# Performance work log

Hardware: AMD Instinct MI355X
Metric: run time of the kernel (lower is better)

Reference implementation:

```python
import jax, jax.numpy as jnp
import numpy as np

N = 20000      # nodes (single node type)
E = 320000     # edges per relation (avg degree 16)
R = 3          # relations / edge types
L = 3          # layers
H = 4          # heads
D = 64         # dim per head (hid_size // n_heads)
IN = 256       # in_size == hid_size
OUT = 128      # out_size
NEG_SLOPE = 0.2


def setup_inputs() -> dict:
    key = jax.random.key(0)
    ks = jax.random.split(key, 8)
    x = jax.random.normal(ks[0], (N, IN), jnp.float32)
    edge_src = jax.random.randint(ks[1], (R, E), 0, N, dtype=jnp.int32)
    edge_dst = jax.random.randint(ks[2], (R, E), 0, N, dtype=jnp.int32)
    W = jax.random.normal(ks[3], (L, R, IN, H * D), jnp.float32) * (1.0 / np.sqrt(IN))
    attn_l = jax.random.normal(ks[4], (L, R, H, D), jnp.float32) * 0.1
    attn_r = jax.random.normal(ks[5], (L, R, H, D), jnp.float32) * 0.1
    bias = jnp.zeros((L, R, H * D), jnp.float32)
    fc_w = jax.random.normal(ks[6], (IN, OUT), jnp.float32) * (1.0 / np.sqrt(IN))
    fc_b = jnp.zeros((OUT,), jnp.float32)
    return dict(x=x, edge_src=edge_src, edge_dst=edge_dst, W=W,
                attn_l=attn_l, attn_r=attn_r, bias=bias, fc_w=fc_w, fc_b=fc_b)


def _gat_conv(h, src, dst, W_r, al, ar, b_r):
    # h: [N, IN] -> feat: [N, H, D]
    feat = (h @ W_r).reshape(N, H, D)
    el = jnp.sum(feat * al, axis=-1)                      # [N, H]
    er = jnp.sum(feat * ar, axis=-1)                      # [N, H]
    e = jax.nn.leaky_relu(el[src] + er[dst], NEG_SLOPE)   # [E, H]
    # segment softmax over incoming edges of each dst node, per head
    m = jax.ops.segment_max(e, dst, num_segments=N)       # [N, H]
    a = jnp.exp(e - m[dst])
    s = jax.ops.segment_sum(a, dst, num_segments=N)       # [N, H]
    alpha = a / s[dst]                                    # [E, H]
    # weighted scatter-add of source features: [N, H, D]
    out = jax.ops.segment_sum(alpha[:, :, None] * feat[src], dst, num_segments=N)
    return out + b_r.reshape(1, H, D)


def reference(x, edge_src, edge_dst, W, attn_l, attn_r, bias, fc_w, fc_b):
    h = x
    for l in range(L):
        acc = jnp.zeros((N, H, D), h.dtype)
        for r in range(R):  # sum-aggregate across relations (HeteroGraphConv aggregate='sum')
            acc = acc + _gat_conv(h, edge_src[r], edge_dst[r],
                                  W[l, r], attn_l[l, r], attn_r[l, r], bias[l, r])
        h = acc.reshape(N, H * D)
        if l != L - 1:
            h = jax.nn.relu(h)  # dropout = identity in eval
    return h @ fc_w + fc_b  # [N, OUT]
```

## Files before the change

kernel.cpp:

```cpp
#include <hip/hip_runtime.h>
#include <math.h>

#define NN 20000
#define EE 320000
#define RR 3
#define LL 3
#define HH 4
#define DD 64
#define CDIM 256
#define OUTD 128
#define NEG 0.2f

typedef float f32x4 __attribute__((ext_vector_type(4)));
typedef short sh8 __attribute__((ext_vector_type(8)));

__device__ __forceinline__ ushort f2bf(float f) {
    union { float f; uint u; } v; v.f = f;
    uint r = (v.u + 0x7FFF + ((v.u >> 16) & 1)) >> 16;
    return (ushort)r;
}
__device__ __forceinline__ float bf2f(ushort u) {
    union { uint u; float f; } v; v.u = ((uint)u) << 16;
    return v.f;
}
__device__ __forceinline__ float bflo(uint p) { return bf2f((ushort)(p & 0xffff)); }
__device__ __forceinline__ float bfhi(uint p) { return bf2f((ushort)(p >> 16)); }


__global__ void zero_ints(int* p, int n) {
    int i = blockIdx.x * blockDim.x + threadIdx.x;
    if (i < n) p[i] = 0;
}

__global__ void count_deg(const int* __restrict__ edge_dst, int* __restrict__ deg) {
    int i = blockIdx.x * blockDim.x + threadIdx.x;
    if (i >= RR * EE) return;
    int r = i / EE;
    atomicAdd(&deg[r * NN + edge_dst[i]], 1);
}

__global__ __launch_bounds__(1024) void scan_kernel(
    const int* __restrict__ deg, int* __restrict__ row_ptr) {
    int r = blockIdx.x;
    const int* d = deg + r * NN;
    int* rp = row_ptr + r * (NN + 1);
    __shared__ int wsum[16];
    int lane = threadIdx.x & 63, wv = threadIdx.x >> 6;
    if (threadIdx.x == 0) rp[0] = 0;
    int carry = 0;
    for (int base = 0; base < NN; base += 1024) {
        int i = base + threadIdx.x;
        int v = (i < NN) ? d[i] : 0;
        int s = v;
        #pragma unroll
        for (int off = 1; off < 64; off <<= 1) {
            int n = __shfl_up(s, off, 64);
            if (lane >= off) s += n;
        }
        if (lane == 63) wsum[wv] = s;
        __syncthreads();
        if (wv == 0) {
            int ws = (lane < 16) ? wsum[lane] : 0;
            #pragma unroll
            for (int off = 1; off < 16; off <<= 1) {
                int n = __shfl_up(ws, off, 64);
                if (lane >= off) ws += n;
            }
            if (lane < 16) wsum[lane] = ws;
        }
        __syncthreads();
        int incl = carry + (wv ? wsum[wv - 1] : 0) + s;
        if (i < NN) rp[i + 1] = incl;
        carry += wsum[15];
        __syncthreads();
    }
}

__global__ void fill_csr(const int* __restrict__ edge_src, const int* __restrict__ edge_dst,
                         const int* __restrict__ row_ptr, int* __restrict__ fill,
                         int* __restrict__ csr_src) {
    int i = blockIdx.x * blockDim.x + threadIdx.x;
    if (i >= RR * EE) return;
    int r = i / EE;
    int dst = edge_dst[i];
    int pos = atomicAdd(&fill[r * NN + dst], 1);
    csr_src[r * EE + row_ptr[r * (NN + 1) + dst] + pos] = edge_src[i];
}


__global__ void cvt_bf16x4(const float* __restrict__ in, ushort* __restrict__ out, int n4) {
    int i = blockIdx.x * blockDim.x + threadIdx.x;
    if (i >= n4) return;
    float4 v = *(const float4*)(in + (size_t)i * 4);
    ushort4 o;
    o.x = f2bf(v.x); o.y = f2bf(v.y); o.z = f2bf(v.z); o.w = f2bf(v.w);
    *(ushort4*)(out + (size_t)i * 4) = o;
}

__global__ void prep_Wt(const float* __restrict__ W, ushort* __restrict__ Wt, int K, int N) {
    __shared__ float tile[32][33];
    int kb = blockIdx.x * 32, nb = blockIdx.y * 32;
    size_t base = (size_t)blockIdx.z * K * N;
    for (int yy = threadIdx.y; yy < 32; yy += 8)
        tile[yy][threadIdx.x] = W[base + (size_t)(kb + yy) * N + nb + threadIdx.x];
    __syncthreads();
    for (int yy = threadIdx.y; yy < 32; yy += 8)
        Wt[base + (size_t)(nb + yy) * K + kb + threadIdx.x] = f2bf(tile[threadIdx.x][yy]);
}


#define TM 128
#define TN 128
#define TK 32
#define LP 40

__global__ __launch_bounds__(256) void gemm_bf16(
    const ushort* __restrict__ A, const ushort* __restrict__ Bt0, void* __restrict__ C0,
    int M, int K, int Ncol, long strideB, long strideC,
    const float* __restrict__ bias, int out_fp32,
    const float* __restrict__ al_all, const float* __restrict__ ar_all,
    float* __restrict__ el_all, float* __restrict__ er_all) {
    __shared__ alignas(16) ushort As[TM * LP];
    __shared__ alignas(16) ushort Bs[TN * LP];
    const ushort* Bt = Bt0 + (size_t)blockIdx.z * strideB;
    int m0 = blockIdx.x * TM, n0 = blockIdx.y * TN;
    int t = threadIdx.x;
    int wave = t >> 6, lane = t & 63;
    int q = lane >> 4, l16 = lane & 15;
    int wrow = (wave >> 1) * 64, wcol = (wave & 1) * 64;

    f32x4 acc[4][4];
    #pragma unroll
    for (int i = 0; i < 4; i++)
        #pragma unroll
        for (int j = 0; j < 4; j++)
            #pragma unroll
            for (int k = 0; k < 4; k++) acc[i][j][k] = 0.f;

    for (int k0 = 0; k0 < K; k0 += TK) {
        #pragma unroll
        for (int s = 0; s < 2; s++) {
            int qid = t + s * 256;
            int row = qid >> 2, kq = (qid & 3) * 8;
            uint4 v = make_uint4(0, 0, 0, 0);
            int gr = m0 + row;
            if (gr < M) v = *(const uint4*)(A + (size_t)gr * K + k0 + kq);
            *(uint4*)(As + row * LP + kq) = v;
        }
        #pragma unroll
        for (int s = 0; s < 2; s++) {
            int qid = t + s * 256;
            int row = qid >> 2, kq = (qid & 3) * 8;
            uint4 v = *(const uint4*)(Bt + (size_t)(n0 + row) * K + k0 + kq);
            *(uint4*)(Bs + row * LP + kq) = v;
        }
        __syncthreads();
        sh8 af[4], bfr[4];
        #pragma unroll
        for (int i = 0; i < 4; i++)
            af[i] = *(const sh8*)(As + (wrow + i * 16 + l16) * LP + q * 8);
        #pragma unroll
        for (int j = 0; j < 4; j++)
            bfr[j] = *(const sh8*)(Bs + (wcol + j * 16 + l16) * LP + q * 8);
        #pragma unroll
        for (int i = 0; i < 4; i++)
            #pragma unroll
            for (int j = 0; j < 4; j++)
                acc[i][j] = __builtin_amdgcn_mfma_f32_16x16x32_bf16(af[i], bfr[j], acc[i][j], 0, 0, 0);
        __syncthreads();
    }

    if (out_fp32) {
        float* C = (float*)C0 + (size_t)blockIdx.z * strideC;
        #pragma unroll
        for (int i = 0; i < 4; i++) {
            #pragma unroll
            for (int reg = 0; reg < 4; reg++) {
                int row = m0 + wrow + i * 16 + q * 4 + reg;
                if (row >= M) continue;
                #pragma unroll
                for (int j = 0; j < 4; j++) {
                    int col = n0 + wcol + j * 16 + l16;
                    float v = acc[i][j][reg];
                    if (bias) v += bias[col];
                    C[(size_t)row * Ncol + col] = v;
                }
            }
        }
    } else {
        ushort* C = (ushort*)C0 + (size_t)blockIdx.z * strideC;
        #pragma unroll
        for (int i = 0; i < 4; i++) {
            #pragma unroll
            for (int reg = 0; reg < 4; reg++) {
                int row = m0 + wrow + i * 16 + q * 4 + reg;
                if (row >= M) continue;
                #pragma unroll
                for (int j = 0; j < 4; j++) {
                    int col = n0 + wcol + j * 16 + l16;
                    C[(size_t)row * Ncol + col] = f2bf(acc[i][j][reg]);
                }
            }
        }
    }

    if (el_all) {
        const float* al = al_all + (size_t)blockIdx.z * CDIM;
        const float* ar = ar_all + (size_t)blockIdx.z * CDIM;
        float* elp = el_all + (size_t)blockIdx.z * NN * HH;
        float* erp = er_all + (size_t)blockIdx.z * NN * HH;
        int head = (n0 + wcol) >> 6;
        float alj[4], arj[4];
        #pragma unroll
        for (int j = 0; j < 4; j++) {
            int gcol = n0 + wcol + j * 16 + l16;
            alj[j] = al[gcol];
            arj[j] = ar[gcol];
        }
        #pragma unroll
        for (int i = 0; i < 4; i++) {
            #pragma unroll
            for (int reg = 0; reg < 4; reg++) {
                int row = m0 + wrow + i * 16 + q * 4 + reg;
                float pl = 0.f, pr = 0.f;
                #pragma unroll
                for (int j = 0; j < 4; j++) {
                    pl = fmaf(acc[i][j][reg], alj[j], pl);
                    pr = fmaf(acc[i][j][reg], arj[j], pr);
                }
                #pragma unroll
                for (int m = 1; m < 16; m <<= 1) {
                    pl += __shfl_xor(pl, m, 64);
                    pr += __shfl_xor(pr, m, 64);
                }
                if (l16 == 0 && row < M) {
                    elp[(size_t)row * HH + head] = pl;
                    erp[(size_t)row * HH + head] = pr;
                }
            }
        }
    }
}

__global__ __launch_bounds__(256) void aggregate_fused(
    const ushort* __restrict__ feat16, const float* __restrict__ el,
    const float* __restrict__ er, const int* __restrict__ row_ptr,
    const int* __restrict__ csr_src, const float* __restrict__ bias,
    ushort* __restrict__ hout, int relu) {
    int wv = threadIdx.x >> 6, lane = threadIdx.x & 63;
    int node = blockIdx.x * 4 + wv;
    if (node >= NN) return;
    int c0 = lane * 4;
    int h = lane >> 4;
    int jj = lane & 3, hh = (lane >> 2) & 3;
    float t0 = 0.f, t1 = 0.f, t2 = 0.f, t3 = 0.f;
    #pragma unroll
    for (int r = 0; r < RR; r++) {
        const int* rp = row_ptr + r * (NN + 1);
        int beg = rp[node], end = rp[node + 1];
        const ushort* fr = feat16 + (size_t)r * NN * CDIM;
        const float* elr = el + (size_t)r * NN * HH;
        float4 ern4 = *(const float4*)(er + ((size_t)r * NN + node) * HH);
        float ern_own = h == 0 ? ern4.x : h == 1 ? ern4.y : h == 2 ? ern4.z : ern4.w;
        float ern_ph = hh == 0 ? ern4.x : hh == 1 ? ern4.y : hh == 2 ? ern4.z : ern4.w;
        const int* cs = csr_src + (size_t)r * EE;
        float p0 = 0.f, p1 = 0.f, p2 = 0.f, p3 = 0.f, ssum = 0.f;
        int e = beg;
        for (; e + 4 <= end; e += 4) {
            int s0 = cs[e], s1 = cs[e + 1], s2 = cs[e + 2], s3 = cs[e + 3];
            int sj = jj == 0 ? s0 : jj == 1 ? s1 : jj == 2 ? s2 : s3;
            float xx = elr[sj * HH + hh] + ern_ph;
            xx = xx > 0.f ? xx : NEG * xx;
            float a = __expf(xx);
            float a0 = __shfl(a, h * 4 + 0, 64);
            float a1 = __shfl(a, h * 4 + 1, 64);
            float a2 = __shfl(a, h * 4 + 2, 64);
            float a3 = __shfl(a, h * 4 + 3, 64);
            uint2 f0 = *(const uint2*)(fr + (size_t)s0 * CDIM + c0);
            uint2 f1 = *(const uint2*)(fr + (size_t)s1 * CDIM + c0);
            uint2 f2 = *(const uint2*)(fr + (size_t)s2 * CDIM + c0);
            uint2 f3 = *(const uint2*)(fr + (size_t)s3 * CDIM + c0);
            ssum += a0 + a1 + a2 + a3;
            p0 = fmaf(a0, bflo(f0.x), p0); p1 = fmaf(a0, bfhi(f0.x), p1);
            p2 = fmaf(a0, bflo(f0.y), p2); p3 = fmaf(a0, bfhi(f0.y), p3);
            p0 = fmaf(a1, bflo(f1.x), p0); p1 = fmaf(a1, bfhi(f1.x), p1);
            p2 = fmaf(a1, bflo(f1.y), p2); p3 = fmaf(a1, bfhi(f1.y), p3);
            p0 = fmaf(a2, bflo(f2.x), p0); p1 = fmaf(a2, bfhi(f2.x), p1);
            p2 = fmaf(a2, bflo(f2.y), p2); p3 = fmaf(a2, bfhi(f2.y), p3);
            p0 = fmaf(a3, bflo(f3.x), p0); p1 = fmaf(a3, bfhi(f3.x), p1);
            p2 = fmaf(a3, bflo(f3.y), p2); p3 = fmaf(a3, bfhi(f3.y), p3);
        }
        for (; e < end; e++) {
            int s = cs[e];
            float x = elr[s * HH + h] + ern_own;
            x = x > 0.f ? x : NEG * x;
            float a = __expf(x);
            uint2 f = *(const uint2*)(fr + (size_t)s * CDIM + c0);
            ssum += a;
            p0 = fmaf(a, bflo(f.x), p0); p1 = fmaf(a, bfhi(f.x), p1);
            p2 = fmaf(a, bflo(f.y), p2); p3 = fmaf(a, bfhi(f.y), p3);
        }
        float is = (end > beg) ? 1.f / ssum : 0.f;
        t0 += p0 * is + bias[r * CDIM + c0];
        t1 += p1 * is + bias[r * CDIM + c0 + 1];
        t2 += p2 * is + bias[r * CDIM + c0 + 2];
        t3 += p3 * is + bias[r * CDIM + c0 + 3];
    }
    if (relu) {
        t0 = fmaxf(t0, 0.f); t1 = fmaxf(t1, 0.f);
        t2 = fmaxf(t2, 0.f); t3 = fmaxf(t3, 0.f);
    }
    uint2 o;
    o.x = (uint)f2bf(t0) | ((uint)f2bf(t1) << 16);
    o.y = (uint)f2bf(t2) | ((uint)f2bf(t3) << 16);
    *(uint2*)(hout + (size_t)node * CDIM + c0) = o;
}


extern "C" void kernel_launch(void* const* d_in, const int* in_sizes, int n_in,
                              void* d_out, int out_size, void* d_ws, size_t ws_size,
                              hipStream_t stream) {
    const float* x        = (const float*)d_in[0];
    const int*   edge_src = (const int*)d_in[1];
    const int*   edge_dst = (const int*)d_in[2];
    const float* W        = (const float*)d_in[3];
    const float* attn_l   = (const float*)d_in[4];
    const float* attn_r   = (const float*)d_in[5];
    const float* bias     = (const float*)d_in[6];
    const float* fc_w     = (const float*)d_in[7];
    const float* fc_b     = (const float*)d_in[8];
    float* out = (float*)d_out;

    char* ws = (char*)d_ws;
    size_t off = 0;
    auto alloc = [&](size_t bytes) {
        void* p = ws + off;
        off = (off + bytes + 255) & ~(size_t)255;
        return p;
    };
    ushort* x16    = (ushort*)alloc((size_t)NN * CDIM * 2);
    ushort* h16    = (ushort*)alloc((size_t)NN * CDIM * 2);
    ushort* feat16 = (ushort*)alloc((size_t)RR * NN * CDIM * 2);
    ushort* Wt16   = (ushort*)alloc((size_t)LL * RR * CDIM * CDIM * 2);
    ushort* fct16  = (ushort*)alloc((size_t)OUTD * CDIM * 2);
    float* el      = (float*)alloc((size_t)RR * NN * HH * 4);
    float* er      = (float*)alloc((size_t)RR * NN * HH * 4);
    int* row_ptr   = (int*)alloc((size_t)RR * (NN + 1) * 4);
    int* csr_src   = (int*)alloc((size_t)RR * EE * 4);
    int* deg       = (int*)alloc((size_t)2 * RR * NN * 4);
    int* fill      = deg + RR * NN;

    zero_ints<<<dim3((2 * RR * NN + 1023) / 1024), dim3(1024), 0, stream>>>(deg, 2 * RR * NN);
    count_deg<<<dim3((RR * EE + 255) / 256), dim3(256), 0, stream>>>(edge_dst, deg);
    scan_kernel<<<dim3(RR), dim3(1024), 0, stream>>>(deg, row_ptr);
    fill_csr<<<dim3((RR * EE + 255) / 256), dim3(256), 0, stream>>>(edge_src, edge_dst, row_ptr, fill, csr_src);

    cvt_bf16x4<<<dim3((NN * CDIM / 4 + 255) / 256), dim3(256), 0, stream>>>(x, x16, NN * CDIM / 4);
    prep_Wt<<<dim3(CDIM / 32, CDIM / 32, LL * RR), dim3(32, 8), 0, stream>>>(W, Wt16, CDIM, CDIM);
    prep_Wt<<<dim3(CDIM / 32, OUTD / 32, 1), dim3(32, 8), 0, stream>>>(fc_w, fct16, CDIM, OUTD);

    const ushort* hin = x16;
    for (int l = 0; l < LL; l++) {
        const ushort* Wl = Wt16 + (size_t)l * RR * CDIM * CDIM;
        dim3 g((NN + TM - 1) / TM, CDIM / TN, RR);
        gemm_bf16<<<g, dim3(256), 0, stream>>>(hin, Wl, feat16, NN, CDIM, CDIM,
                                               (long)CDIM * CDIM, (long)NN * CDIM, nullptr, 0,
                                               attn_l + (size_t)l * RR * CDIM,
                                               attn_r + (size_t)l * RR * CDIM, el, er);
        aggregate_fused<<<dim3(NN / 4), dim3(256), 0, stream>>>(
            feat16, el, er, row_ptr, csr_src, bias + (size_t)l * RR * CDIM,
            h16, (l != LL - 1) ? 1 : 0);
        hin = h16;
    }
    dim3 gf((NN + TM - 1) / TM, OUTD / TN, 1);
    gemm_bf16<<<gf, dim3(256), 0, stream>>>(h16, fct16, out, NN, CDIM, OUTD,
                                            0, 0, fc_b, 1, nullptr, nullptr, nullptr, nullptr);
}
```

Before: 535.6 us.

## Use row-pointer cursor for CSR fill and per-lane attention logits in aggregate

CSR construction now copies row_ptr into a cursor array and atomically increments it directly, which drops the separate fill counter, the extra row_ptr load and half of the zeroing. In the aggregation kernel, each lane now computes its own head's four edge logits with four el loads and four exps, replacing the earlier scheme where lanes computed one logit each and shared them via shuffles. This removes the shuffles and the select logic but adds redundant el loads and exp work per lane.

```diff
diff --git a/kernel.cpp b/kernel.cpp
--- a/kernel.cpp
+++ b/kernel.cpp
@@ -77,14 +77,13 @@
 }
 
 __global__ void fill_csr(const int* __restrict__ edge_src, const int* __restrict__ edge_dst,
-                         const int* __restrict__ row_ptr, int* __restrict__ fill,
-                         int* __restrict__ csr_src) {
+                         int* __restrict__ cursor, int* __restrict__ csr_src) {
     int i = blockIdx.x * blockDim.x + threadIdx.x;
     if (i >= RR * EE) return;
     int r = i / EE;
     int dst = edge_dst[i];
-    int pos = atomicAdd(&fill[r * NN + dst], 1);
-    csr_src[r * EE + row_ptr[r * (NN + 1) + dst] + pos] = edge_src[i];
+    int pos = atomicAdd(&cursor[r * (NN + 1) + dst], 1);
+    csr_src[r * EE + pos] = edge_src[i];
 }
 
 
@@ -252,7 +251,6 @@
     if (node >= NN) return;
     int c0 = lane * 4;
     int h = lane >> 4;
-    int jj = lane & 3, hh = (lane >> 2) & 3;
     float t0 = 0.f, t1 = 0.f, t2 = 0.f, t3 = 0.f;
     #pragma unroll
     for (int r = 0; r < RR; r++) {
@@ -260,26 +258,26 @@
         int beg = rp[node], end = rp[node + 1];
         const ushort* fr = feat16 + (size_t)r * NN * CDIM;
         const float* elr = el + (size_t)r * NN * HH;
-        float4 ern4 = *(const float4*)(er + ((size_t)r * NN + node) * HH);
-        float ern_own = h == 0 ? ern4.x : h == 1 ? ern4.y : h == 2 ? ern4.z : ern4.w;
-        float ern_ph = hh == 0 ? ern4.x : hh == 1 ? ern4.y : hh == 2 ? ern4.z : ern4.w;
+        float ern = er[((size_t)r * NN + node) * HH + h];
         const int* cs = csr_src + (size_t)r * EE;
         float p0 = 0.f, p1 = 0.f, p2 = 0.f, p3 = 0.f, ssum = 0.f;
         int e = beg;
         for (; e + 4 <= end; e += 4) {
             int s0 = cs[e], s1 = cs[e + 1], s2 = cs[e + 2], s3 = cs[e + 3];
-            int sj = jj == 0 ? s0 : jj == 1 ? s1 : jj == 2 ? s2 : s3;
-            float xx = elr[sj * HH + hh] + ern_ph;
-            xx = xx > 0.f ? xx : NEG * xx;
-            float a = __expf(xx);
-            float a0 = __shfl(a, h * 4 + 0, 64);
-            float a1 = __shfl(a, h * 4 + 1, 64);
-            float a2 = __shfl(a, h * 4 + 2, 64);
-            float a3 = __shfl(a, h * 4 + 3, 64);
+            float x0 = elr[s0 * HH + h];
+            float x1 = elr[s1 * HH + h];
+            float x2 = elr[s2 * HH + h];
+            float x3 = elr[s3 * HH + h];
             uint2 f0 = *(const uint2*)(fr + (size_t)s0 * CDIM + c0);
             uint2 f1 = *(const uint2*)(fr + (size_t)s1 * CDIM + c0);
             uint2 f2 = *(const uint2*)(fr + (size_t)s2 * CDIM + c0);
             uint2 f3 = *(const uint2*)(fr + (size_t)s3 * CDIM + c0);
+            x0 += ern; x1 += ern; x2 += ern; x3 += ern;
+            x0 = x0 > 0.f ? x0 : NEG * x0;
+            x1 = x1 > 0.f ? x1 : NEG * x1;
+            x2 = x2 > 0.f ? x2 : NEG * x2;
+            x3 = x3 > 0.f ? x3 : NEG * x3;
+            float a0 = __expf(x0), a1 = __expf(x1), a2 = __expf(x2), a3 = __expf(x3);
             ssum += a0 + a1 + a2 + a3;
             p0 = fmaf(a0, bflo(f0.x), p0); p1 = fmaf(a0, bfhi(f0.x), p1);
             p2 = fmaf(a0, bflo(f0.y), p2); p3 = fmaf(a0, bfhi(f0.y), p3);
@@ -292,7 +290,7 @@
         }
         for (; e < end; e++) {
             int s = cs[e];
-            float x = elr[s * HH + h] + ern_own;
+            float x = elr[s * HH + h] + ern;
             x = x > 0.f ? x : NEG * x;
             float a = __expf(x);
             uint2 f = *(const uint2*)(fr + (size_t)s * CDIM + c0);
@@ -346,14 +344,17 @@
     float* el      = (float*)alloc((size_t)RR * NN * HH * 4);
     float* er      = (float*)alloc((size_t)RR * NN * HH * 4);
     int* row_ptr   = (int*)alloc((size_t)RR * (NN + 1) * 4);
+    int* cursor    = (int*)alloc((size_t)RR * (NN + 1) * 4);
     int* csr_src   = (int*)alloc((size_t)RR * EE * 4);
-    int* deg       = (int*)alloc((size_t)2 * RR * NN * 4);
-    int* fill      = deg + RR * NN;
-
-    zero_ints<<<dim3((2 * RR * NN + 1023) / 1024), dim3(1024), 0, stream>>>(deg, 2 * RR * NN);
+    int* deg       = (int*)alloc((size_t)RR * NN * 4);
+
+    zero_ints<<<dim3((RR * NN + 1023) / 1024), dim3(1024), 0, stream>>>(deg, RR * NN);
     count_deg<<<dim3((RR * EE + 255) / 256), dim3(256), 0, stream>>>(edge_dst, deg);
     scan_kernel<<<dim3(RR), dim3(1024), 0, stream>>>(deg, row_ptr);
-    fill_csr<<<dim3((RR * EE + 255) / 256), dim3(256), 0, stream>>>(edge_src, edge_dst, row_ptr, fill, csr_src);
+    hipMemcpyAsync(cursor, row_ptr, (size_t)RR * (NN + 1) * 4,
+                   hipMemcpyDeviceToDevice, stream);
+    fill_csr<<<dim3((RR * EE + 255) / 256), dim3(256), 0, stream>>>(
+        edge_src, edge_dst, cursor, csr_src);
 
     cvt_bf16x4<<<dim3((NN * CDIM / 4 + 255) / 256), dim3(256), 0, stream>>>(x, x16, NN * CDIM / 4);
     prep_Wt<<<dim3(CDIM / 32, CDIM / 32, LL * RR), dim3(32, 8), 0, stream>>>(W, Wt16, CDIM, CDIM);
```

Result: no change. 534.6 us (-0.2%).
